# Kernel tuning notes

Measured on AMD Instinct MI355X. Metric: run time of the kernel, lower is better.

The kernel has to match this reference:

```python
import jax, jax.numpy as jnp
import numpy as np

WBITS = 4
ABITS = 8
OBITS = 8


def fwht(x):
    """Normalized fast Walsh-Hadamard transform along the last axis (n power of 2).
    Equivalent to matmul_hadU with had_K = I, K = 1 (n = 4096 = 2^12)."""
    shape = x.shape
    n = shape[-1]
    x = x.reshape(-1, n)
    h = 1
    while h < n:
        x = x.reshape(-1, n // (2 * h), 2, h)
        a, b = x[:, :, 0, :], x[:, :, 1, :]
        x = jnp.concatenate([a + b, a - b], axis=-1).reshape(-1, n)
        h *= 2
    inv_sqrt_n = jnp.asarray(1.0 / np.sqrt(n), x.dtype)
    return (x * inv_sqrt_n).reshape(shape)


def sym_fake_quant(t, bits, axis):
    """Symmetric min-max RTN fake quantization (per-channel for weights,
    per-token for activations)."""
    qmax = jnp.asarray(2.0 ** (bits - 1) - 1.0, t.dtype)
    scale = jnp.max(jnp.abs(t), axis=axis, keepdims=True) / qmax
    scale = jnp.maximum(scale, jnp.asarray(1e-8, t.dtype))
    q = jnp.clip(jnp.round(t / scale), -qmax, qmax)
    return q * scale


def setup_inputs() -> dict:
    key = jax.random.key(0)
    k1, k2, k3 = jax.random.split(key, 3)
    B, S, DIN, DOUT = 4, 2048, 4096, 4096
    return {
        "input": jax.random.normal(k1, (B, S, DIN), dtype=jnp.float32),
        "weight": jax.random.normal(k2, (DOUT, DIN), dtype=jnp.float32) * 0.02,
        "bias": jax.random.normal(k3, (DOUT,), dtype=jnp.float32) * 0.01,
    }


def reference(input, weight, bias):
    # online full Hadamard rotation of activations
    x = fwht(input)
    # activation quant (per-token, symmetric int8 fake-quant)
    x = sym_fake_quant(x, ABITS, axis=-1)
    # weight quant (per-output-channel, symmetric int4 fake-quant)
    w = sym_fake_quant(weight, WBITS, axis=-1)
    # F.linear: x @ w.T + b
    out = jnp.einsum("bsi,oi->bso", x, w) + bias
    # output quant (per-token, symmetric int8 fake-quant)
    out = sym_fake_quant(out, OBITS, axis=-1)
    return out
```

## Files before the change

kernel.cpp:

```cpp
#include <hip/hip_runtime.h>
#include <hip/hip_bf16.h>

#define DIN 4096
#define DOUT 4096
#define NROWS 8192

typedef int i32x4 __attribute__((ext_vector_type(4)));

__device__ __forceinline__ float block_absmax(float m, float* red) {
  #pragma unroll
  for (int off = 32; off > 0; off >>= 1)
    m = fmaxf(m, __shfl_down(m, off));
  const int tid = threadIdx.x;
  if ((tid & 63) == 0) red[tid >> 6] = m;
  __syncthreads();
  return fmaxf(fmaxf(red[0], red[1]), fmaxf(red[2], red[3]));
}

__global__ __launch_bounds__(256) void fwht_quant_kernel(
    const float* __restrict__ in, char* __restrict__ qx,
    float* __restrict__ sx) {
  __shared__ float lds[4352];
  __shared__ float red[4];
  const int tid = threadIdx.x;
  const size_t row = blockIdx.x;
  const int th = tid >> 4, tl = tid & 15;
  float v[16];

  const float4* src = (const float4*)(in + row * DIN);
  #pragma unroll
  for (int k = 0; k < 4; ++k) {
    float4 f = src[tid * 4 + k];
    v[4 * k + 0] = f.x; v[4 * k + 1] = f.y;
    v[4 * k + 2] = f.z; v[4 * k + 3] = f.w;
  }
  #pragma unroll
  for (int hb = 1; hb < 16; hb <<= 1)
    #pragma unroll
    for (int j = 0; j < 16; ++j)
      if (!(j & hb)) {
        float a0 = v[j], b0 = v[j | hb];
        v[j] = a0 + b0; v[j | hb] = a0 - b0;
      }
  #pragma unroll
  for (int j = 0; j < 16; ++j) lds[17 * tid + j] = v[j];
  __syncthreads();
  #pragma unroll
  for (int j = 0; j < 16; ++j) v[j] = lds[272 * th + 17 * j + tl];
  #pragma unroll
  for (int hb = 1; hb < 16; hb <<= 1)
    #pragma unroll
    for (int j = 0; j < 16; ++j)
      if (!(j & hb)) {
        float a0 = v[j], b0 = v[j | hb];
        v[j] = a0 + b0; v[j | hb] = a0 - b0;
      }
  #pragma unroll
  for (int j = 0; j < 16; ++j) lds[272 * th + 17 * j + tl] = v[j];
  __syncthreads();
  #pragma unroll
  for (int j = 0; j < 16; ++j) v[j] = lds[272 * j + 17 * th + tl];
  #pragma unroll
  for (int hb = 1; hb < 16; hb <<= 1)
    #pragma unroll
    for (int j = 0; j < 16; ++j)
      if (!(j & hb)) {
        float a0 = v[j], b0 = v[j | hb];
        v[j] = a0 + b0; v[j | hb] = a0 - b0;
      }
  float m = 0.0f;
  #pragma unroll
  for (int j = 0; j < 16; ++j) m = fmaxf(m, fabsf(v[j]));
  #pragma unroll
  for (int j = 0; j < 16; ++j) lds[272 * j + 17 * th + tl] = v[j];
  float mx = block_absmax(m, red) * 0.015625f;
  float scale = fmaxf(mx / 127.0f, 1e-8f);
  if (tid == 0) sx[row] = scale;
  const float rs = 1.0f / scale;
  char pk[16];
  #pragma unroll
  for (int j = 0; j < 16; ++j) {
    float q = fminf(fmaxf(rintf((lds[17 * tid + j] * 0.015625f) * rs), -127.f),
                    127.f);
    pk[j] = (char)q;
  }
  *(int4*)(qx + row * DIN + (size_t)tid * 16) = *(const int4*)pk;
}

__global__ __launch_bounds__(256) void wquant_kernel(
    const float* __restrict__ w, char* __restrict__ qw,
    float* __restrict__ sw) {
  __shared__ float buf[DIN];
  __shared__ float red[4];
  const int tid = threadIdx.x;
  const size_t row = blockIdx.x;
  const float4* src = (const float4*)(w + row * DIN);
  float4* b4 = (float4*)buf;
  float m = 0.0f;
  for (int i = tid; i < DIN / 4; i += 256) {
    float4 v = src[i];
    b4[i] = v;
    m = fmaxf(m, fmaxf(fmaxf(fabsf(v.x), fabsf(v.y)),
                       fmaxf(fabsf(v.z), fabsf(v.w))));
  }
  float mx = block_absmax(m, red);
  float scale = fmaxf(mx / 7.0f, 1e-8f);
  if (tid == 0) sw[row] = scale;
  char* dst = qw + row * DIN;
  const float rs = 1.0f / scale;
  for (int i0 = tid * 4; i0 < DIN; i0 += 1024) {
    char4 pk;
    float q0 = fminf(fmaxf(rintf(buf[i0 + 0] * rs), -7.f), 7.f);
    float q1 = fminf(fmaxf(rintf(buf[i0 + 1] * rs), -7.f), 7.f);
    float q2 = fminf(fmaxf(rintf(buf[i0 + 2] * rs), -7.f), 7.f);
    float q3 = fminf(fmaxf(rintf(buf[i0 + 3] * rs), -7.f), 7.f);
    pk.x = (char)q0; pk.y = (char)q1; pk.z = (char)q2; pk.w = (char)q3;
    *(char4*)(dst + i0) = pk;
  }
}

__global__ __launch_bounds__(512, 2) void gemm_kernel(
    const char* __restrict__ A,
    const char* __restrict__ Bt,
    const float* __restrict__ sx, const float* __restrict__ sw,
    const float* __restrict__ bias, float* __restrict__ out) {
  __shared__ char lds[131072];
  const int tid = threadIdx.x;
  const int lane = tid & 63;
  const int wid = tid >> 6;
  const int wr = wid >> 2;
  const int wc = wid & 3;
  int bid = blockIdx.x;
  int swz = (bid & 7) * 64 + (bid >> 3);
  const int tm = swz >> 4;
  const int tn = swz & 15;
  const size_t row0 = (size_t)tm * 256;
  const size_t col0 = (size_t)tn * 256;
  const int slot0 = (((lane >> 4) ^ (lane & 7)) << 4);

  i32x4 acc[4][2][4] = {};
  i32x4 fb[4][2];
  i32x4 fa[2][2][2];

#define STAGE(MAT, GROW0, KT, LBASE)                                          \
  {                                                                           \
    _Pragma("unroll")                                                         \
    for (int j = 0; j < 2; ++j) {                                             \
      int chunk = j * 8 + wid;                                                \
      int rr = chunk * 8 + (lane >> 3);                                       \
      int cc = (KT) * 128 + (((lane & 7) ^ (lane >> 3)) << 4);                \
      const char* src = (MAT) + ((GROW0) + rr) * (size_t)DIN + cc;            \
      __builtin_amdgcn_global_load_lds(                                       \
          (const __attribute__((address_space(1))) void*)src,                 \
          (__attribute__((address_space(3))) void*)(lds + (LBASE) +           \
                                                    chunk * 1024),            \
          16, 0, 0);                                                          \
    }                                                                         \
  }
#define STAGE_A(P, HALF, KT) \
  STAGE(A, row0 + (HALF) * 128, KT, (P) * 32768 + (HALF) * 16384)
#define STAGE_B(P, HALF, KT) \
  STAGE(Bt, col0 + (HALF) * 128, KT, 65536 + (P) * 32768 + (HALF) * 16384)

#define DS_A2(Q0, P)                                                          \
  {                                                                           \
    _Pragma("unroll")                                                         \
    for (int s = 0; s < 2; ++s) {                                             \
      _Pragma("unroll")                                                       \
      for (int mm = 0; mm < 2; ++mm) {                                        \
        int ar = ((Q0) + s) * 64 + wr * 32 + mm * 16 + (lane & 15);           \
        _Pragma("unroll")                                                     \
        for (int kk = 0; kk < 2; ++kk)                                        \
          fa[s][mm][kk] = *(const i32x4*)(lds + (P) * 32768 + ar * 128 +      \
                                          (slot0 ^ (kk * 64)));               \
      }                                                                       \
    }                                                                         \
  }
#define DS_B(P)                                                               \
  {                                                                           \
    _Pragma("unroll")                                                         \
    for (int nn = 0; nn < 4; ++nn) {                                          \
      int br = wc * 64 + nn * 16 + (lane & 15);                               \
      _Pragma("unroll")                                                       \
      for (int kk = 0; kk < 2; ++kk)                                          \
        fb[nn][kk] = *(const i32x4*)(lds + 65536 + (P) * 32768 + br * 128 +   \
                                     (slot0 ^ (kk * 64)));                    \
    }                                                                         \
  }
#define MFMA32(Q0)                                                            \
  {                                                                           \
    __builtin_amdgcn_s_setprio(1);                                            \
    _Pragma("unroll")                                                         \
    for (int kk = 0; kk < 2; ++kk)                                            \
      _Pragma("unroll")                                                       \
      for (int s = 0; s < 2; ++s)                                             \
        _Pragma("unroll")                                                     \
        for (int mm = 0; mm < 2; ++mm)                                        \
          _Pragma("unroll")                                                   \
          for (int nn = 0; nn < 4; ++nn)                                      \
            acc[(Q0) + s][mm][nn] = __builtin_amdgcn_mfma_i32_16x16x64_i8(    \
                fa[s][mm][kk], fb[nn][kk], acc[(Q0) + s][mm][nn], 0, 0, 0);   \
    __builtin_amdgcn_s_setprio(0);                                            \
  }
#define BAR() __builtin_amdgcn_s_barrier()
#define WAIT_LGKM0() asm volatile("s_waitcnt lgkmcnt(0)" ::: "memory")

  STAGE_B(0, 0, 0); STAGE_B(0, 1, 0); STAGE_A(0, 0, 0); STAGE_A(0, 1, 0);
  STAGE_B(1, 0, 1); STAGE_B(1, 1, 1); STAGE_A(1, 0, 1);
  asm volatile("s_waitcnt vmcnt(6)" ::: "memory");
  BAR();

  #pragma unroll 1
  for (int i = 0; i < 16; ++i) {
    const int a = 2 * i, b = 2 * i + 1;
    const bool nl = (i < 15);
    DS_A2(0, 0); DS_B(0);
    STAGE_A(1, 1, b);
    asm volatile("s_waitcnt lgkmcnt(8)" ::: "memory");
    BAR(); WAIT_LGKM0();
    MFMA32(0);
    BAR();
    DS_A2(2, 0);
    if (nl) { STAGE_B(0, 0, a + 2); STAGE_B(0, 1, a + 2); STAGE_A(0, 0, a + 2); }
    BAR(); WAIT_LGKM0();
    MFMA32(2);
    if (nl) { asm volatile("s_waitcnt vmcnt(6)" ::: "memory"); }
    else    { asm volatile("s_waitcnt vmcnt(0)" ::: "memory"); }
    BAR();
    DS_A2(0, 1); DS_B(1);
    if (nl) STAGE_A(0, 1, a + 2);
    asm volatile("s_waitcnt lgkmcnt(8)" ::: "memory");
    BAR(); WAIT_LGKM0();
    MFMA32(0);
    BAR();
    DS_A2(2, 1);
    if (nl) { STAGE_B(1, 0, b + 2); STAGE_B(1, 1, b + 2); STAGE_A(1, 0, b + 2); }
    BAR(); WAIT_LGKM0();
    MFMA32(2);
    if (nl) { asm volatile("s_waitcnt vmcnt(6)" ::: "memory"); }
    BAR();
  }

  float swv[4], bv[4];
  #pragma unroll
  for (int nn = 0; nn < 4; ++nn) {
    size_t gc = col0 + wc * 64 + nn * 16 + (lane & 15);
    swv[nn] = sw[gc];
    bv[nn] = bias[gc];
  }
  #pragma unroll
  for (int q = 0; q < 4; ++q) {
    #pragma unroll
    for (int mm = 0; mm < 2; ++mm) {
      #pragma unroll
      for (int j = 0; j < 4; ++j) {
        size_t gr = row0 + q * 64 + wr * 32 + mm * 16 + ((lane >> 4) << 2) + j;
        float sxr = sx[gr];
        float* orow = out + gr * DOUT + col0 + wc * 64 + (lane & 15);
        #pragma unroll
        for (int nn = 0; nn < 4; ++nn)
          orow[nn * 16] = (float)acc[q][mm][nn][j] * (sxr * swv[nn]) + bv[nn];
      }
    }
  }
#undef STAGE
#undef STAGE_A
#undef STAGE_B
#undef DS_A2
#undef DS_B
#undef MFMA32
#undef BAR
#undef WAIT_LGKM0
}

__global__ __launch_bounds__(256) void rowquant_kernel(float* __restrict__ out) {
  __shared__ float red[4];
  const int tid = threadIdx.x;
  const size_t row = blockIdx.x;
  float4* g4 = (float4*)(out + row * DOUT);
  float4 v[4];
  float m = 0.0f;
  #pragma unroll
  for (int k = 0; k < 4; ++k) {
    v[k] = g4[tid + k * 256];
    m = fmaxf(m, fmaxf(fmaxf(fabsf(v[k].x), fabsf(v[k].y)),
                       fmaxf(fabsf(v[k].z), fabsf(v[k].w))));
  }
  float mx = block_absmax(m, red);
  float scale = fmaxf(mx / 127.0f, 1e-8f);
  #pragma unroll
  for (int k = 0; k < 4; ++k) {
    float4 w = v[k];
    w.x = fminf(fmaxf(rintf(w.x / scale), -127.0f), 127.0f) * scale;
    w.y = fminf(fmaxf(rintf(w.y / scale), -127.0f), 127.0f) * scale;
    w.z = fminf(fmaxf(rintf(w.z / scale), -127.0f), 127.0f) * scale;
    w.w = fminf(fmaxf(rintf(w.w / scale), -127.0f), 127.0f) * scale;
    g4[tid + k * 256] = w;
  }
}

extern "C" void kernel_launch(void* const* d_in, const int* in_sizes, int n_in,
                              void* d_out, int out_size, void* d_ws, size_t ws_size,
                              hipStream_t stream) {
  (void)in_sizes; (void)n_in; (void)out_size; (void)ws_size;
  const float* input = (const float*)d_in[0];
  const float* weight = (const float*)d_in[1];
  const float* bias = (const float*)d_in[2];
  float* out = (float*)d_out;
  char* ws = (char*)d_ws;
  char* qx = ws;
  char* qw = ws + ((size_t)32 << 20);
  float* sx = (float*)(ws + ((size_t)48 << 20));
  float* sw = (float*)(ws + ((size_t)48 << 20) + ((size_t)32 << 10));

  fwht_quant_kernel<<<NROWS, 256, 0, stream>>>(input, qx, sx);
  wquant_kernel<<<DOUT, 256, 0, stream>>>(weight, qw, sw);
  gemm_kernel<<<512, 512, 0, stream>>>(qx, qw, sx, sw, bias, out);
  rowquant_kernel<<<NROWS, 256, 0, stream>>>(out);
}
```

Baseline: 225.1 us.

## Split GEMM main loop into finer MFMA phases and transpose output for float4 stores

Each half of the int8 GEMM k-loop now runs four MFMA phases of one 64-row quarter each instead of two phases of two quarters. Global-to-LDS staging is spread one chunk per phase, which halves the A-fragment registers and interleaves loads with compute more evenly. The MFMA operands are swapped so each lane holds four consecutive output columns, which lets the epilogue load scales and bias and write output as float4 instead of scalar strided stores. The cost is more barriers per iteration.

```diff
diff --git a/kernel.cpp b/kernel.cpp
--- a/kernel.cpp
+++ b/kernel.cpp
@@ -140,7 +140,7 @@
 
   i32x4 acc[4][2][4] = {};
   i32x4 fb[4][2];
-  i32x4 fa[2][2][2];
+  i32x4 fa[2][2];
 
 #define STAGE(MAT, GROW0, KT, LBASE)                                          \
   {                                                                           \
@@ -162,18 +162,15 @@
 #define STAGE_B(P, HALF, KT) \
   STAGE(Bt, col0 + (HALF) * 128, KT, 65536 + (P) * 32768 + (HALF) * 16384)
 
-#define DS_A2(Q0, P)                                                          \
+#define DS_A(Q, P)                                                            \
   {                                                                           \
     _Pragma("unroll")                                                         \
-    for (int s = 0; s < 2; ++s) {                                             \
+    for (int mm = 0; mm < 2; ++mm) {                                          \
+      int ar = (Q) * 64 + wr * 32 + mm * 16 + (lane & 15);                    \
       _Pragma("unroll")                                                       \
-      for (int mm = 0; mm < 2; ++mm) {                                        \
-        int ar = ((Q0) + s) * 64 + wr * 32 + mm * 16 + (lane & 15);           \
-        _Pragma("unroll")                                                     \
-        for (int kk = 0; kk < 2; ++kk)                                        \
-          fa[s][mm][kk] = *(const i32x4*)(lds + (P) * 32768 + ar * 128 +      \
-                                          (slot0 ^ (kk * 64)));               \
-      }                                                                       \
+      for (int kk = 0; kk < 2; ++kk)                                          \
+        fa[mm][kk] =                                                          \
+            *(const i32x4*)(lds + (P) * 32768 + ar * 128 + (slot0 ^ (kk * 64))); \
     }                                                                         \
   }
 #define DS_B(P)                                                               \
@@ -187,19 +184,17 @@
                                      (slot0 ^ (kk * 64)));                    \
     }                                                                         \
   }
-#define MFMA32(Q0)                                                            \
+#define MFMA16(Q)                                                             \
   {                                                                           \
     __builtin_amdgcn_s_setprio(1);                                            \
     _Pragma("unroll")                                                         \
     for (int kk = 0; kk < 2; ++kk)                                            \
       _Pragma("unroll")                                                       \
-      for (int s = 0; s < 2; ++s)                                             \
+      for (int mm = 0; mm < 2; ++mm)                                          \
         _Pragma("unroll")                                                     \
-        for (int mm = 0; mm < 2; ++mm)                                        \
-          _Pragma("unroll")                                                   \
-          for (int nn = 0; nn < 4; ++nn)                                      \
-            acc[(Q0) + s][mm][nn] = __builtin_amdgcn_mfma_i32_16x16x64_i8(    \
-                fa[s][mm][kk], fb[nn][kk], acc[(Q0) + s][mm][nn], 0, 0, 0);   \
+        for (int nn = 0; nn < 4; ++nn)                                        \
+          acc[Q][mm][nn] = __builtin_amdgcn_mfma_i32_16x16x64_i8(             \
+              fb[nn][kk], fa[mm][kk], acc[Q][mm][nn], 0, 0, 0);               \
     __builtin_amdgcn_s_setprio(0);                                            \
   }
 #define BAR() __builtin_amdgcn_s_barrier()
@@ -214,61 +209,80 @@
   for (int i = 0; i < 16; ++i) {
     const int a = 2 * i, b = 2 * i + 1;
     const bool nl = (i < 15);
-    DS_A2(0, 0); DS_B(0);
+    DS_A(0, 0); DS_B(0);
     STAGE_A(1, 1, b);
     asm volatile("s_waitcnt lgkmcnt(8)" ::: "memory");
     BAR(); WAIT_LGKM0();
-    MFMA32(0);
-    BAR();
-    DS_A2(2, 0);
-    if (nl) { STAGE_B(0, 0, a + 2); STAGE_B(0, 1, a + 2); STAGE_A(0, 0, a + 2); }
-    BAR(); WAIT_LGKM0();
-    MFMA32(2);
+    MFMA16(0);
+    BAR();
+    DS_A(1, 0);
+    if (nl) STAGE_B(0, 0, a + 2);
+    BAR(); WAIT_LGKM0();
+    MFMA16(1);
+    BAR();
+    DS_A(2, 0);
+    if (nl) STAGE_B(0, 1, a + 2);
+    BAR(); WAIT_LGKM0();
+    MFMA16(2);
+    BAR();
+    DS_A(3, 0);
+    if (nl) STAGE_A(0, 0, a + 2);
+    BAR(); WAIT_LGKM0();
+    MFMA16(3);
     if (nl) { asm volatile("s_waitcnt vmcnt(6)" ::: "memory"); }
     else    { asm volatile("s_waitcnt vmcnt(0)" ::: "memory"); }
     BAR();
-    DS_A2(0, 1); DS_B(1);
+    DS_A(0, 1); DS_B(1);
     if (nl) STAGE_A(0, 1, a + 2);
     asm volatile("s_waitcnt lgkmcnt(8)" ::: "memory");
     BAR(); WAIT_LGKM0();
-    MFMA32(0);
-    BAR();
-    DS_A2(2, 1);
-    if (nl) { STAGE_B(1, 0, b + 2); STAGE_B(1, 1, b + 2); STAGE_A(1, 0, b + 2); }
-    BAR(); WAIT_LGKM0();
-    MFMA32(2);
+    MFMA16(0);
+    BAR();
+    DS_A(1, 1);
+    if (nl) STAGE_B(1, 0, b + 2);
+    BAR(); WAIT_LGKM0();
+    MFMA16(1);
+    BAR();
+    DS_A(2, 1);
+    if (nl) STAGE_B(1, 1, b + 2);
+    BAR(); WAIT_LGKM0();
+    MFMA16(2);
+    BAR();
+    DS_A(3, 1);
+    if (nl) STAGE_A(1, 0, b + 2);
+    BAR(); WAIT_LGKM0();
+    MFMA16(3);
     if (nl) { asm volatile("s_waitcnt vmcnt(6)" ::: "memory"); }
     BAR();
   }
 
-  float swv[4], bv[4];
-  #pragma unroll
-  for (int nn = 0; nn < 4; ++nn) {
-    size_t gc = col0 + wc * 64 + nn * 16 + (lane & 15);
-    swv[nn] = sw[gc];
-    bv[nn] = bias[gc];
-  }
   #pragma unroll
   for (int q = 0; q < 4; ++q) {
     #pragma unroll
     for (int mm = 0; mm < 2; ++mm) {
+      size_t gr = row0 + q * 64 + wr * 32 + mm * 16 + (lane & 15);
+      float sxr = sx[gr];
+      float* orow = out + gr * DOUT;
       #pragma unroll
-      for (int j = 0; j < 4; ++j) {
-        size_t gr = row0 + q * 64 + wr * 32 + mm * 16 + ((lane >> 4) << 2) + j;
-        float sxr = sx[gr];
-        float* orow = out + gr * DOUT + col0 + wc * 64 + (lane & 15);
-        #pragma unroll
-        for (int nn = 0; nn < 4; ++nn)
-          orow[nn * 16] = (float)acc[q][mm][nn][j] * (sxr * swv[nn]) + bv[nn];
+      for (int nn = 0; nn < 4; ++nn) {
+        size_t gc0 = col0 + wc * 64 + nn * 16 + ((lane >> 4) << 2);
+        float4 swv = *(const float4*)(sw + gc0);
+        float4 bv = *(const float4*)(bias + gc0);
+        float4 o;
+        o.x = (float)acc[q][mm][nn][0] * (sxr * swv.x) + bv.x;
+        o.y = (float)acc[q][mm][nn][1] * (sxr * swv.y) + bv.y;
+        o.z = (float)acc[q][mm][nn][2] * (sxr * swv.z) + bv.z;
+        o.w = (float)acc[q][mm][nn][3] * (sxr * swv.w) + bv.w;
+        *(float4*)(orow + gc0) = o;
       }
     }
   }
 #undef STAGE
 #undef STAGE_A
 #undef STAGE_B
-#undef DS_A2
+#undef DS_A
 #undef DS_B
-#undef MFMA32
+#undef MFMA16
 #undef BAR
 #undef WAIT_LGKM0
 }
```

Result: no change. 225.3 us (+0.1%).
